# Kernel optimization log

Hardware: AMD Instinct MI355X
Metric: run time of the kernel (lower is better)

Reference implementation:

```python
import jax, jax.numpy as jnp
import numpy as np

T, C, NH, NL, NP = 5, 192, 4, 5, 4
DH = C // NH

def leaky(x):
    return jnp.where(x >= 0, x, 0.1 * x)

def conv2d(x, w, b, padding=1, dilation=1):
    out = jax.lax.conv_general_dilated(
        x, w, window_strides=(1, 1),
        padding=[(padding, padding), (padding, padding)],
        rhs_dilation=(dilation, dilation),
        dimension_numbers=('NCHW', 'OIHW', 'NCHW'))
    return out + b[None, :, None, None]

def grid_sample_border(img, gx, gy):
    # align_corners=True, padding_mode='border'; gx/gy normalized [-1,1], shape (B,H,W)
    B, Cc, H, W = img.shape
    x = jnp.clip((gx + 1.0) * 0.5 * (W - 1), 0.0, W - 1)
    y = jnp.clip((gy + 1.0) * 0.5 * (H - 1), 0.0, H - 1)
    x0 = jnp.floor(x); y0 = jnp.floor(y)
    wx = (x - x0).reshape(B, 1, -1); wy = (y - y0).reshape(B, 1, -1)
    flat = img.reshape(B, Cc, H * W)
    def g(yi, xi):
        xi = jnp.clip(xi, 0, W - 1).astype(jnp.int32)
        yi = jnp.clip(yi, 0, H - 1).astype(jnp.int32)
        return jnp.take_along_axis(flat, (yi * W + xi).reshape(B, 1, -1), axis=2)
    out = (g(y0, x0) * (1 - wx) * (1 - wy) + g(y0, x0 + 1) * wx * (1 - wy)
         + g(y0 + 1, x0) * (1 - wx) * wy + g(y0 + 1, x0 + 1) * wx * wy)
    return out.reshape(B, Cc, H, W)

def warp(x, flo):
    B, _, H, W = x.shape
    xx = jnp.arange(W, dtype=jnp.float32)[None, :] * jnp.ones((H, 1), jnp.float32)
    yy = jnp.arange(H, dtype=jnp.float32)[:, None] * jnp.ones((1, W), jnp.float32)
    gx = 2.0 * (xx[None] + flo[:, 0]) / max(W - 1, 1) - 1.0
    gy = 2.0 * (yy[None] + flo[:, 1]) / max(H - 1, 1) - 1.0
    return grid_sample_border(x, gx, gy)

def deform_sample(v_img, loc):
    # v_img (N,D,H,W); loc (N,Q,P,2) in [0,1]; bilinear, zeros padding, align_corners=False
    N, D, H, W = v_img.shape
    Q, P = loc.shape[1], loc.shape[2]
    x = loc[..., 0] * W - 0.5
    y = loc[..., 1] * H - 0.5
    x0 = jnp.floor(x); y0 = jnp.floor(y)
    wx = (x - x0).reshape(N, 1, -1); wy = (y - y0).reshape(N, 1, -1)
    flat = v_img.reshape(N, D, H * W)
    def g(yi, xi):
        valid = ((xi >= 0) & (xi <= W - 1) & (yi >= 0) & (yi <= H - 1)).astype(v_img.dtype)
        xi_c = jnp.clip(xi, 0, W - 1).astype(jnp.int32)
        yi_c = jnp.clip(yi, 0, H - 1).astype(jnp.int32)
        return jnp.take_along_axis(flat, (yi_c * W + xi_c).reshape(N, 1, -1), axis=2) * valid.reshape(N, 1, -1)
    out = (g(y0, x0) * (1 - wx) * (1 - wy) + g(y0, x0 + 1) * wx * (1 - wy)
         + g(y0 + 1, x0) * (1 - wx) * wy + g(y0 + 1, x0 + 1) * wx * wy)
    return out.reshape(N, D, Q, P)

def _forward(frame, srcframe, flow_forward, flow_backward,
             w_qk, b_qk, w_v, b_v, w_vproj, b_vproj, w_off, b_off,
             w_attn, b_attn, w_out, b_out, w_ff, b_ff,
             w_ffn1, b_ffn1, w_ffn2, b_ffn2):
    b, t, c, h, w = frame.shape
    ff01, ff12 = flow_forward[:, 0], flow_forward[:, 1]
    fb32, fb43 = flow_backward[:, 2], flow_backward[:, 3]
    ff02 = ff01 + warp(ff12, ff01)
    fb42 = fb43 + warp(fb32, fb43)
    warp02 = warp(frame[:, 0], ff02)
    warp12 = warp(frame[:, 1], ff12)
    warp32 = warp(frame[:, 3], fb32)
    warp42 = warp(frame[:, 4], fb42)
    qk_in = jnp.concatenate([warp02, warp12, frame[:, 2], warp32, warp42,
                             flow_forward.reshape(b, -1, h, w),
                             flow_backward.reshape(b, -1, h, w)], axis=1)
    queries = leaky(conv2d(qk_in, w_qk, b_qk)).reshape(b, t, c, h, w)
    value = leaky(conv2d(frame.reshape(b, t * c, h, w), w_v, b_v)).reshape(b, t, c, h, w)

    Lq = t * h * w
    q_tok = queries.transpose(0, 1, 3, 4, 2).reshape(b, Lq, c)
    v_tok = value.transpose(0, 1, 3, 4, 2).reshape(b, Lq, c)
    v_proj = (v_tok @ w_vproj.T + b_vproj).reshape(b, t, h * w, NH, DH)

    offs = (q_tok @ w_off.T + b_off).reshape(b, Lq, NH, NL, NP, 2)
    aw = (q_tok @ w_attn.T + b_attn).reshape(b, Lq, NH, NL * NP)
    aw = jax.nn.softmax(aw, axis=-1).reshape(b, Lq, NH, NL, NP)

    # reference points (all valid ratios are ones): ((x+0.5)/W, (y+0.5)/H)
    rx = (jnp.arange(w, dtype=frame.dtype) + 0.5) / w
    ry = (jnp.arange(h, dtype=frame.dtype) + 0.5) / h
    ref = jnp.stack(jnp.meshgrid(rx, ry, indexing='xy'), axis=-1).reshape(h * w, 2)
    ref = jnp.tile(ref, (t, 1))  # (Lq, 2)

    norm = jnp.array([w, h], dtype=frame.dtype)
    # flow-guided per-level displacement toward the center frame (level 2)
    zero = jnp.zeros_like(ff12)
    flows = jnp.stack([ff02, ff12, zero, fb32, fb42], axis=1)  # (b,NL,2,h,w)
    flow_norm = (flows / norm[None, None, :, None, None]).transpose(0, 1, 3, 4, 2).reshape(b, NL, h * w, 2)
    flow_norm = jnp.tile(flow_norm.transpose(0, 2, 1, 3), (1, t, 1, 1))  # (b,Lq,NL,2)

    loc = (ref[None, :, None, None, None, :]
           + offs / norm[None, None, None, None, None, :]
           + flow_norm[:, :, None, :, None, :])  # (b,Lq,NH,NL,NP,2)

    acc = jnp.zeros((b * NH, DH, Lq), dtype=frame.dtype)
    for l in range(NL):
        v_l = v_proj[:, l].transpose(0, 2, 3, 1).reshape(b * NH, DH, h, w)
        loc_l = loc[:, :, :, l].transpose(0, 2, 1, 3, 4).reshape(b * NH, Lq, NP, 2)
        samp = deform_sample(v_l, loc_l)  # (b*NH, DH, Lq, NP)
        w_l = aw[:, :, :, l].transpose(0, 2, 1, 3).reshape(b * NH, 1, Lq, NP)
        acc = acc + (samp * w_l).sum(-1)
    attn = acc.reshape(b, NH, DH, Lq).transpose(0, 3, 1, 2).reshape(b, Lq, c)
    attn = attn @ w_out.T + b_out

    out = attn.reshape(b, t, h, w, c).transpose(0, 1, 4, 2, 3).reshape(b * t, c, h, w)
    out = conv2d(out, w_ff, b_ff)
    out = out.reshape(b, t, c, h, w) + frame
    seq_in = jnp.concatenate([out.reshape(b * t, c, h, w), srcframe.reshape(b * t, c, h, w)], axis=1)
    ffn = conv2d(seq_in, w_ffn1, b_ffn1, padding=2, dilation=2)
    ffn = conv2d(leaky(ffn), w_ffn2, b_ffn2)
    out = out.reshape(b * t, c, h, w) + ffn
    return out.reshape(b, t, c, h, w)

def setup_inputs():
    key = jax.random.key(0)
    ks = jax.random.split(key, 16)
    B, H, W = 2, 64, 64
    s = 0.02
    d = {}
    d['frame'] = jax.random.normal(ks[0], (B, T, C, H, W), jnp.float32)
    d['srcframe'] = jax.random.normal(ks[1], (B, T, C, H, W), jnp.float32)
    d['flow_forward'] = jax.random.normal(ks[2], (B, 4, 2, H, W), jnp.float32)
    d['flow_backward'] = jax.random.normal(ks[3], (B, 4, 2, H, W), jnp.float32)
    cin_qk = T * C + 4 * (T - 1)
    d['w_qk'] = jax.random.normal(ks[4], (T * C, cin_qk, 3, 3), jnp.float32) * s
    d['b_qk'] = jnp.zeros((T * C,), jnp.float32)
    d['w_v'] = jax.random.normal(ks[5], (T * C, T * C, 3, 3), jnp.float32) * s
    d['b_v'] = jnp.zeros((T * C,), jnp.float32)
    d['w_vproj'] = jax.random.normal(ks[6], (C, C), jnp.float32) * s
    d['b_vproj'] = jnp.zeros((C,), jnp.float32)
    d['w_off'] = jax.random.normal(ks[7], (NH * NL * NP * 2, C), jnp.float32) * s
    d['b_off'] = jax.random.normal(ks[8], (NH * NL * NP * 2,), jnp.float32)
    d['w_attn'] = jax.random.normal(ks[9], (NH * NL * NP, C), jnp.float32) * s
    d['b_attn'] = jnp.zeros((NH * NL * NP,), jnp.float32)
    d['w_out'] = jax.random.normal(ks[10], (C, C), jnp.float32) * s
    d['b_out'] = jnp.zeros((C,), jnp.float32)
    d['w_ff'] = jax.random.normal(ks[11], (C, C, 3, 3), jnp.float32) * s
    d['b_ff'] = jnp.zeros((C,), jnp.float32)
    d['w_ffn1'] = jax.random.normal(ks[12], (C, 2 * C, 3, 3), jnp.float32) * s
    d['b_ffn1'] = jnp.zeros((C,), jnp.float32)
    d['w_ffn2'] = jax.random.normal(ks[13], (C, C, 3, 3), jnp.float32) * s
    d['b_ffn2'] = jnp.zeros((C,), jnp.float32)
    return d

def reference(frame, srcframe, flow_forward, flow_backward, w_qk, b_qk, w_v, b_v, w_vproj, b_vproj, w_off, b_off, w_attn, b_attn, w_out, b_out, w_ff, b_ff, w_ffn1, b_ffn1, w_ffn2, b_ffn2):
    out = _forward(frame, srcframe, flow_forward, flow_backward, w_qk, b_qk, w_v, b_v, w_vproj, b_vproj, w_off, b_off, w_attn, b_attn, w_out, b_out, w_ff, b_ff, w_ffn1, b_ffn1, w_ffn2, b_ffn2)
    return (out, srcframe)
```

## Files before the change

### kernel.cpp

```cpp
#include <hip/hip_runtime.h>


#define HWPX 4096
#define PPXN 4624
#define LQ   20480

typedef __attribute__((ext_vector_type(8))) short  short8;
typedef __attribute__((ext_vector_type(4))) short  short4v;
typedef __attribute__((ext_vector_type(4))) float  f32x4;

__device__ __forceinline__ unsigned short f2bf(float f) {
    unsigned u = __float_as_uint(f);
    unsigned r = (u + 0x7FFF + ((u >> 16) & 1)) >> 16;
    return (unsigned short)r;
}
__device__ __forceinline__ float bf2f(unsigned short s) {
    return __uint_as_float(((unsigned)s) << 16);
}

__device__ __forceinline__ void gl_lds16(const unsigned short* g, unsigned short* l) {
    __builtin_amdgcn_global_load_lds(
        (const __attribute__((address_space(1))) unsigned int*)g,
        (__attribute__((address_space(3))) unsigned int*)l, 16, 0, 0);
}

__device__ __forceinline__ float bsample(const float* __restrict__ p, float sx, float sy) {
    sx = fminf(fmaxf(sx, 0.f), 63.f);
    sy = fminf(fmaxf(sy, 0.f), 63.f);
    float x0 = floorf(sx), y0 = floorf(sy);
    int ix0 = (int)x0, iy0 = (int)y0;
    int ix1 = ix0 < 63 ? ix0 + 1 : 63;
    int iy1 = iy0 < 63 ? iy0 + 1 : 63;
    float wx = sx - x0, wy = sy - y0;
    float v00 = p[iy0*64+ix0], v01 = p[iy0*64+ix1];
    float v10 = p[iy1*64+ix0], v11 = p[iy1*64+ix1];
    return (v00*(1.f-wx) + v01*wx)*(1.f-wy) + (v10*(1.f-wx) + v11*wx)*wy;
}

__global__ __launch_bounds__(256) void k_flow(const float* __restrict__ ff,
                                              const float* __restrict__ fb,
                                              float* __restrict__ flows) {
    int i = blockIdx.x*256 + threadIdx.x;
    int b = i >> 12, pix = i & 4095;
    int x = pix & 63, y = pix >> 6;
    const float* ff01 = ff + (size_t)(b*4+0)*2*HWPX;
    const float* ff12 = ff + (size_t)(b*4+1)*2*HWPX;
    const float* fb32 = fb + (size_t)(b*4+2)*2*HWPX;
    const float* fb43 = fb + (size_t)(b*4+3)*2*HWPX;
    float* F = flows + (size_t)b*5*2*HWPX;
    float ax = ff01[pix], ay = ff01[HWPX+pix];
    float sx = bsample(ff12,      (float)x+ax, (float)y+ay);
    float sy = bsample(ff12+HWPX, (float)x+ax, (float)y+ay);
    F[0*2*HWPX + pix]        = ax + sx;
    F[0*2*HWPX + HWPX + pix] = ay + sy;
    F[1*2*HWPX + pix]        = ff12[pix];
    F[1*2*HWPX + HWPX + pix] = ff12[HWPX+pix];
    F[2*2*HWPX + pix]        = 0.f;
    F[2*2*HWPX + HWPX + pix] = 0.f;
    F[3*2*HWPX + pix]        = fb32[pix];
    F[3*2*HWPX + HWPX + pix] = fb32[HWPX+pix];
    float bx = fb43[pix], by = fb43[HWPX+pix];
    float tx = bsample(fb32,      (float)x+bx, (float)y+by);
    float ty = bsample(fb32+HWPX, (float)x+bx, (float)y+by);
    F[4*2*HWPX + pix]        = bx + tx;
    F[4*2*HWPX + HWPX + pix] = by + ty;
}

__global__ void k_qkin(const unsigned short* __restrict__ Pv,
                       const float* __restrict__ ff, const float* __restrict__ fb,
                       const float* __restrict__ flows,
                       unsigned short* __restrict__ Pqk)
{
    int ppx = blockIdx.x*64 + threadIdx.x;
    if (ppx >= PPXN) return;
    int b = blockIdx.z;
    int c8 = (blockIdx.y*4 + threadIdx.y)*8;
    unsigned short* dst = Pqk + ((size_t)b*PPXN + ppx)*992 + c8;
    int py = ppx/68, pxc = ppx - py*68;
    short8 o = {};
    if (py >= 2 && py < 66 && pxc >= 2 && pxc < 66 && c8 < 976) {
        int y = py-2, x = pxc-2, pix = (y<<6)+x;
        if (c8 >= 960) {
            #pragma unroll
            for (int j = 0; j < 8; ++j) {
                int k = c8 - 960 + j;
                float v = (k < 8) ? ff[((size_t)b*8 + k)*HWPX + pix]
                                  : fb[((size_t)b*8 + k - 8)*HWPX + pix];
                o[j] = (short)f2bf(v);
            }
        } else {
            const unsigned short* Pvb = Pv + (size_t)b*PPXN*960;
            int slot = c8/192;
            if (slot == 2) {
                o = *(const short8*)(Pvb + (size_t)ppx*960 + c8);
            } else {
                const float* F = flows + ((size_t)(b*5 + slot)*2)*HWPX;
                float sx = fminf(fmaxf((float)x + F[pix], 0.f), 63.f);
                float sy = fminf(fmaxf((float)y + F[HWPX + pix], 0.f), 63.f);
                float x0 = floorf(sx), y0 = floorf(sy);
                int ix0 = (int)x0, iy0 = (int)y0;
                int ix1 = ix0 < 63 ? ix0+1 : 63, iy1 = iy0 < 63 ? iy0+1 : 63;
                float wx = sx - x0, wy = sy - y0;
                float w00 = (1.f-wx)*(1.f-wy), w01 = wx*(1.f-wy);
                float w10 = (1.f-wx)*wy,       w11 = wx*wy;
                short8 v00 = *(const short8*)(Pvb + ((size_t)((iy0+2)*68 + ix0+2))*960 + c8);
                short8 v01 = *(const short8*)(Pvb + ((size_t)((iy0+2)*68 + ix1+2))*960 + c8);
                short8 v10 = *(const short8*)(Pvb + ((size_t)((iy1+2)*68 + ix0+2))*960 + c8);
                short8 v11 = *(const short8*)(Pvb + ((size_t)((iy1+2)*68 + ix1+2))*960 + c8);
                #pragma unroll
                for (int j = 0; j < 8; ++j) {
                    float v = bf2f((unsigned short)v00[j])*w00 + bf2f((unsigned short)v01[j])*w01
                            + bf2f((unsigned short)v10[j])*w10 + bf2f((unsigned short)v11[j])*w11;
                    o[j] = (short)f2bf(v);
                }
            }
        }
    }
    *(short8*)dst = o;
}

__global__ void t_pad(const float* __restrict__ in, unsigned short* __restrict__ outb,
                      int CI, int PITCH, int COFF)
{
    int ppx = blockIdx.x*64 + threadIdx.x;
    if (ppx >= PPXN) return;
    int img = blockIdx.z;
    int c8 = (blockIdx.y*4 + threadIdx.y)*8;
    unsigned short* dst = outb + ((size_t)img*PPXN + ppx)*PITCH;
    int py = ppx/68, pxc = ppx - py*68;
    if (py < 2 || py >= 66 || pxc < 2 || pxc >= 66) {
        short8 z = {};
        *(short8*)(dst + c8) = z;
        if (COFF) *(short8*)(dst + COFF + c8) = z;
        return;
    }
    int pix = ((py-2)<<6) + (pxc-2);
    short8 o;
    #pragma unroll
    for (int j = 0; j < 8; ++j)
        o[j] = (short)f2bf(in[((size_t)img*CI + c8 + j)*HWPX + pix]);
    *(short8*)(dst + COFF + c8) = o;
}

__global__ __launch_bounds__(256) void t_zb(unsigned short* __restrict__ b0,
                                            unsigned short* __restrict__ b1) {
    int id = blockIdx.x*256 + threadIdx.x;
    int ppx = id / 24, c8 = (id - ppx*24) * 8;
    if (ppx >= PPXN) return;
    int py = ppx/68, pxc = ppx - py*68;
    if (py >= 2 && py < 66 && pxc >= 2 && pxc < 66) return;
    int y = blockIdx.y;
    unsigned short* buf = (y < 10) ? b0 : b1;
    int img = (y < 10) ? y : y - 10;
    short8 z = {};
    *(short8*)(buf + ((size_t)img*PPXN + ppx)*192 + c8) = z;
}

__global__ __launch_bounds__(256) void t_wT(const float* __restrict__ w,
                                            unsigned short* __restrict__ wT,
                                            int CI, int NKB) {
    int cotile = blockIdx.x, kblk = blockIdx.y;
    int tid = threadIdx.x & 255;
    unsigned short* dst = wT + ((size_t)(cotile*NKB + kblk))*18432;
    #pragma unroll
    for (int it = 0; it < 9; ++it) {
        int idx = it*256 + tid;
        int tap = idx >> 8, sub = idx & 255;
        int cg = sub >> 6, co = sub & 63;
        int cog = cotile*64 + co;
        int ci0 = kblk*32 + cg*8;
        short8 v;
        #pragma unroll
        for (int j = 0; j < 8; ++j) {
            int ci = ci0 + j;
            v[j] = (ci < CI) ? (short)f2bf(w[((size_t)cog*CI + ci)*9 + tap]) : (short)0;
        }
        *(short8*)(dst + (size_t)idx*8) = v;
    }
}

__global__ __launch_bounds__(256) void t_wg(const float* __restrict__ w1,
                                            const float* __restrict__ w2,
                                            unsigned short* __restrict__ wg,
                                            int co_split, int CO) {
    int cotile = blockIdx.x;
    int tid = threadIdx.x & 255;
    unsigned short* dst = wg + (size_t)cotile*12288;
    #pragma unroll
    for (int it = 0; it < 6; ++it) {
        int idx = it*256 + tid;
        int kblk = idx >> 8, sub = idx & 255;
        int cg = sub >> 6, co = sub & 63;
        int cog = cotile*64 + co;
        int ci0 = kblk*32 + cg*8;
        short8 v = {};
        if (cog < CO) {
            const float* row = (cog < co_split) ? w1 + (size_t)cog*192
                                                : w2 + (size_t)(cog - co_split)*192;
            #pragma unroll
            for (int j = 0; j < 8; ++j) v[j] = (short)f2bf(row[ci0 + j]);
        }
        *(short8*)(dst + (size_t)idx*8) = v;
    }
}

template<int ROWS, int DIL, int OUTK, bool LEAKY, int RESK>
__global__ __launch_bounds__(256, 2) void k_conv(
    const unsigned short* __restrict__ P0, const unsigned short* __restrict__ P1,
    int CIP0, int CIP1, int NKB0, int NKB1,
    const unsigned short* __restrict__ wT0, const unsigned short* __restrict__ wT1,
    const float* __restrict__ bias0, const float* __restrict__ bias1,
    const float* __restrict__ resF, const unsigned short* __restrict__ resB, int resPitch,
    float* __restrict__ outF,
    unsigned short* __restrict__ outB0, unsigned short* __restrict__ outB1,
    int outPitch, int outCoff, int njobs)
{
    constexpr int RR     = ROWS*4 + 2*DIL;
    constexpr int XP     = 64 + 2*DIL;
    constexpr int PLANE  = RR*XP*16;
    constexpr int NCH    = RR*XP*4;
    constexpr int NXS    = (NCH + 255)/256;
    constexpr int TILEPX = ROWS*4*64;
    constexpr int SMEM_K = 4*PLANE + 36864;
    constexpr int SMEM_E = (OUTK <= 1) ? TILEPX*72*2 : 0;
    constexpr int SMEMSZ = SMEM_K > SMEM_E ? SMEM_K : SMEM_E;
    __shared__ __align__(16) unsigned char smem[SMEMSZ];
    unsigned char*  s_x = smem;
    unsigned short* s_w = (unsigned short*)(smem + 4*PLANE);

    int tid = threadIdx.x & 255;
    int gx = gridDim.x, gy = gridDim.y, gz = gridDim.z;
    int lin = blockIdx.x + gx*(blockIdx.y + gy*blockIdx.z);
    int tot = gx*gy*gz;
    if ((tot & 7) == 0) { int q = tot >> 3; lin = (lin & 7)*q + (lin >> 3); }
    int cotile = lin % gx; int rem = lin / gx;
    int ytile = rem % gy;  int z = rem / gy;

    int sel = (njobs == 2) ? (z >> 1) : 0;
    int img = (njobs == 2) ? (z & 1)  : z;
    const unsigned short* P  = sel ? P1  : P0;
    const unsigned short* wT = sel ? wT1 : wT0;
    const float* bias        = sel ? bias1 : bias0;
    unsigned short* outB     = sel ? outB1 : outB0;
    int CIP = sel ? CIP1 : CIP0;
    int NKB = sel ? NKB1 : NKB0;

    int y0 = ytile * (ROWS*4);
    const unsigned short* Pi = P + (size_t)img*PPXN*CIP;
    int w = tid >> 6, lane = tid & 63, lm = lane & 15, cig = lane >> 4;

    auto stage_x = [&](int kb) {
        int k0 = kb*32;
        #pragma unroll
        for (int it = 0; it < NXS; ++it) {
            int li = it*256 + tid;
            if (li < NCH) {
                int p = li / (RR*XP), rm = li - p*(RR*XP);
                int r = rm / XP, c = rm - r*XP;
                gl_lds16(Pi + ((size_t)((y0 + 2 - DIL + r)*68 + c + 2 - DIL))*CIP + k0 + p*8,
                         (unsigned short*)(s_x + li*16));
            }
        }
    };
    auto stage_w = [&](int kb) {
        const unsigned short* ws = wT + ((size_t)(cotile*NKB + kb))*18432;
        #pragma unroll
        for (int it = 0; it < 9; ++it)
            gl_lds16(ws + (size_t)(it*256+tid)*8, &s_w[(it*256+tid)*8]);
    };

    stage_x(0); stage_w(0);
    __syncthreads();

    f32x4 acc[4][ROWS*4] = {};
    for (int kb = 0; kb < NKB; ++kb) {
        __builtin_amdgcn_s_setprio(1);
        #pragma unroll
        for (int t = 0; t < 9; ++t) {
            int ky = t/3, kx = t - ky*3;
            short8 A[4];
            #pragma unroll
            for (int mb = 0; mb < 4; ++mb)
                A[mb] = *(const short8*)&s_w[((t*4 + cig)*64 + mb*16 + lm)*8];
            #pragma unroll
            for (int s = 0; s < ROWS; ++s) {
                short8 Bf[4];
                #pragma unroll
                for (int nc = 0; nc < 4; ++nc)
                    Bf[nc] = *(const short8*)&s_x[cig*PLANE +
                               ((w*ROWS + s + ky*DIL)*XP + nc*16 + lm + kx*DIL)*16];
                #pragma unroll
                for (int mb = 0; mb < 4; ++mb)
                    #pragma unroll
                    for (int nc = 0; nc < 4; ++nc)
                        acc[mb][s*4+nc] = __builtin_amdgcn_mfma_f32_16x16x32_bf16(
                            A[mb], Bf[nc], acc[mb][s*4+nc], 0, 0, 0);
            }
        }
        __builtin_amdgcn_s_setprio(0);
        __syncthreads();
        if (kb + 1 < NKB) { stage_x(kb+1); stage_w(kb+1); }
        __syncthreads();
    }

    if (OUTK == 0 || OUTK == 1) {
        unsigned short* epi = (unsigned short*)smem;
        #pragma unroll
        for (int mb = 0; mb < 4; ++mb) {
            int cob = cotile*64 + mb*16 + cig*4;
            int col = mb*16 + cig*4;
            #pragma unroll
            for (int s = 0; s < ROWS; ++s) {
                int lr = w*ROWS + s;
                #pragma unroll
                for (int nc = 0; nc < 4; ++nc) {
                    int x = nc*16 + lm;
                    int px_l = lr*64 + x;
                    int gpx = y0*64 + px_l;
                    short4v sv;
                    #pragma unroll
                    for (int r = 0; r < 4; ++r) {
                        float v = acc[mb][s*4+nc][r] + bias[cob + r];
                        if (LEAKY) v = v >= 0.f ? v : 0.1f*v;
                        if (RESK == 1) v += resF[((size_t)img*192 + cob + r)*HWPX + gpx];
                        sv[r] = (short)f2bf(v);
                    }
                    *(short4v*)&epi[px_l*72 + col] = sv;
                }
            }
        }
        __syncthreads();
        constexpr int NCPY = TILEPX/32;
        int slot = (OUTK == 0) ? (cotile*64)/192 : 0;
        int ccb  = (OUTK == 0) ? (cotile*64)%192 : (cotile*64 + outCoff);
        #pragma unroll
        for (int it2 = 0; it2 < NCPY; ++it2) {
            int li = it2*256 + tid;
            int px_l = li >> 3, sub = li & 7;
            short8 v = *(const short8*)&epi[px_l*72 + sub*8];
            int gpx = y0*64 + px_l;
            if (OUTK == 0) {
                *(short8*)(outB + ((size_t)(img*5 + slot)*HWPX + gpx)*192 + ccb + sub*8) = v;
            } else {
                int ppx = ((gpx>>6)+2)*68 + (gpx&63) + 2;
                *(short8*)(outB0 + ((size_t)img*PPXN + ppx)*outPitch + ccb + sub*8) = v;
            }
        }
    } else {
        #pragma unroll
        for (int mb = 0; mb < 4; ++mb) {
            int cob = cotile*64 + mb*16 + cig*4;
            #pragma unroll
            for (int s = 0; s < ROWS; ++s) {
                int y = y0 + w*ROWS + s;
                #pragma unroll
                for (int nc = 0; nc < 4; ++nc) {
                    int x = nc*16 + lm;
                    int px = (y<<6) + x;
                    int ppx = (y+2)*68 + x + 2;
                    short4v rv;
                    if (RESK == 2)
                        rv = *(const short4v*)(resB + ((size_t)img*PPXN + ppx)*resPitch + cob);
                    #pragma unroll
                    for (int r = 0; r < 4; ++r) {
                        float v = acc[mb][s*4+nc][r] + bias[cob + r];
                        if (LEAKY) v = v >= 0.f ? v : 0.1f*v;
                        if (RESK == 1) v += resF[((size_t)img*192 + cob + r)*HWPX + px];
                        if (RESK == 2) v += bf2f((unsigned short)rv[r]);
                        outF[((size_t)img*192 + cob + r)*HWPX + px] = v;
                    }
                }
            }
        }
    }
}

template<int GMODE>
__global__ __launch_bounds__(256) void k_gemmm(
    const unsigned short* __restrict__ X, const unsigned short* __restrict__ WG,
    const float* __restrict__ b1, const float* __restrict__ b2,
    float* __restrict__ o1, float* __restrict__ o2, unsigned short* __restrict__ ob)
{
    __shared__ unsigned char  s_x[2][4*4096];
    __shared__ unsigned short s_w[12288];
    int tid = threadIdx.x & 255;
    int cotile = blockIdx.x, pxt = blockIdx.y, img = blockIdx.z;
    int px0 = pxt*256;
    const unsigned short* Xi = X + (size_t)img*HWPX*192;
    #pragma unroll
    for (int it = 0; it < 6; ++it)
        gl_lds16(WG + (size_t)cotile*12288 + (it*256+tid)*8, &s_w[(it*256+tid)*8]);
    short8 xr[4];
    #pragma unroll
    for (int it = 0; it < 4; ++it)
        xr[it] = *(const short8*)(Xi + (size_t)(px0 + tid)*192 + it*8);
    #pragma unroll
    for (int it = 0; it < 4; ++it)
        *(short8*)&s_x[0][it*4096 + tid*16] = xr[it];
    __syncthreads();
    int w = tid >> 6, lane = tid & 63, lm = lane & 15, cig = lane >> 4;
    f32x4 acc[4][4] = {};
    int xb = 0;
    for (int kb = 0; kb < 6; ++kb) {
        bool pf = (kb < 5);
        if (pf) {
            int k0 = (kb+1)*32;
            #pragma unroll
            for (int it = 0; it < 4; ++it)
                xr[it] = *(const short8*)(Xi + (size_t)(px0 + tid)*192 + k0 + it*8);
        }
        short8 A[4], Bf[4];
        #pragma unroll
        for (int nb = 0; nb < 4; ++nb)
            Bf[nb] = *(const short8*)&s_x[xb][cig*4096 + (w*64 + nb*16 + lm)*16];
        #pragma unroll
        for (int mb = 0; mb < 4; ++mb)
            A[mb] = *(const short8*)&s_w[((kb*4 + cig)*64 + mb*16 + lm)*8];
        #pragma unroll
        for (int mb = 0; mb < 4; ++mb)
            #pragma unroll
            for (int nb = 0; nb < 4; ++nb)
                acc[mb][nb] = __builtin_amdgcn_mfma_f32_16x16x32_bf16(
                    A[mb], Bf[nb], acc[mb][nb], 0, 0, 0);
        if (pf) {
            #pragma unroll
            for (int it = 0; it < 4; ++it)
                *(short8*)&s_x[xb^1][it*4096 + tid*16] = xr[it];
        }
        __syncthreads();
        xb ^= 1;
    }
    int b = img/5, t = img - b*5;
    #pragma unroll
    for (int mb = 0; mb < 4; ++mb) {
        int cob = cotile*64 + mb*16 + cig*4;
        if (GMODE == 1 && cob >= 240) continue;
        #pragma unroll
        for (int nb = 0; nb < 4; ++nb) {
            int px = px0 + w*64 + nb*16 + lm;
            float vv[4];
            #pragma unroll
            for (int r = 0; r < 4; ++r) {
                float bv;
                if (GMODE == 1) bv = (cob + r < 160) ? b1[cob+r] : b2[cob+r-160];
                else bv = b1[cob + r];
                vv[r] = acc[mb][nb][r] + bv;
            }
            if (GMODE == 0) {
                int h = cob/48, d = cob - h*48;
                short4v s;
                #pragma unroll
                for (int r = 0; r < 4; ++r) s[r] = (short)f2bf(vv[r]);
                *(short4v*)(ob + (((size_t)img*4 + h)*HWPX + px)*48 + d) = s;
            } else if (GMODE == 1) {
                #pragma unroll
                for (int r = 0; r < 4; ++r) {
                    int co = cob + r;
                    if (co < 160) o1[((size_t)b*160 + co)*LQ + t*HWPX + px] = vv[r];
                    else          o2[((size_t)b*80 + co-160)*LQ + t*HWPX + px] = vv[r];
                }
            } else {
                int ppx = ((px>>6)+2)*68 + (px&63) + 2;
                short4v s;
                #pragma unroll
                for (int r = 0; r < 4; ++r) s[r] = (short)f2bf(vv[r]);
                *(short4v*)(ob + ((size_t)img*PPXN + ppx)*192 + cob) = s;
            }
        }
    }
}

__device__ __forceinline__ void addtap(float* acc, const unsigned short* __restrict__ src, float w) {
    const short8* s8 = (const short8*)src;
    #pragma unroll
    for (int q = 0; q < 6; ++q) {
        short8 v = s8[q];
        #pragma unroll
        for (int j = 0; j < 8; ++j)
            acc[q*8+j] += w * bf2f((unsigned short)v[j]);
    }
}

__global__ __launch_bounds__(256) void k_sample(
    const unsigned short* __restrict__ vp, const float* __restrict__ offs,
    const float* __restrict__ aw, const float* __restrict__ flows,
    unsigned short* __restrict__ accout)
{
    int blk = blockIdx.x;
    int b = blk / 320, sub = blk - b*320;
    int h = threadIdx.x >> 6;
    int lq = sub*64 + (threadIdx.x & 63);
    int pix = lq & 4095;
    int x = pix & 63, y = pix >> 6;
    const float* offp = offs + ((size_t)b*160 + h*40)*LQ + lq;
    const float* awp  = aw   + ((size_t)b*80  + h*20)*LQ + lq;
    float e[20];
    float m = -1e30f;
    #pragma unroll
    for (int j = 0; j < 20; ++j) { e[j] = awp[(size_t)j*LQ]; m = fmaxf(m, e[j]); }
    float ssum = 0.f;
    #pragma unroll
    for (int j = 0; j < 20; ++j) { e[j] = __expf(e[j]-m); ssum += e[j]; }
    float inv = 1.f/ssum;

    float acc[48];
    #pragma unroll
    for (int d = 0; d < 48; ++d) acc[d] = 0.f;

    for (int l = 0; l < 5; ++l) {
        float fx = flows[((size_t)(b*5+l)*2+0)*HWPX + pix];
        float fy = flows[((size_t)(b*5+l)*2+1)*HWPX + pix];
        const unsigned short* vpl = vp + ((size_t)(b*5+l)*4 + h)*HWPX*48;
        #pragma unroll
        for (int p = 0; p < 4; ++p) {
            int o = l*4 + p;
            float ox = offp[(size_t)(2*o)*LQ];
            float oy = offp[(size_t)(2*o+1)*LQ];
            float wv = e[o]*inv;
            float sx = (float)x + ox + fx;
            float sy = (float)y + oy + fy;
            float x0f = floorf(sx), y0f = floorf(sy);
            float wx = sx - x0f, wy = sy - y0f;
            int ix0 = (int)x0f, iy0 = (int)y0f;
            float w00 = wv*(1.f-wx)*(1.f-wy), w01 = wv*wx*(1.f-wy);
            float w10 = wv*(1.f-wx)*wy,       w11 = wv*wx*wy;
            bool vx0 = (ix0 >= 0)  && (ix0 <= 63);
            bool vx1 = (ix0 >= -1) && (ix0 <= 62);
            bool vy0 = (iy0 >= 0)  && (iy0 <= 63);
            bool vy1 = (iy0 >= -1) && (iy0 <= 62);
            if (vy0 && vx0) addtap(acc, vpl + (size_t)(iy0*64 + ix0)*48,       w00);
            if (vy0 && vx1) addtap(acc, vpl + (size_t)(iy0*64 + ix0 + 1)*48,   w01);
            if (vy1 && vx0) addtap(acc, vpl + (size_t)((iy0+1)*64 + ix0)*48,   w10);
            if (vy1 && vx1) addtap(acc, vpl + (size_t)((iy0+1)*64 + ix0+1)*48, w11);
        }
    }
    unsigned short* dst = accout + ((size_t)b*LQ + lq)*192 + h*48;
    #pragma unroll
    for (int q = 0; q < 6; ++q) {
        short8 s;
        #pragma unroll
        for (int j = 0; j < 8; ++j) s[j] = (short)f2bf(acc[q*8+j]);
        *(short8*)(dst + q*8) = s;
    }
}


extern "C" void kernel_launch(void* const* d_in, const int* in_sizes, int n_in,
                              void* d_out, int out_size, void* d_ws, size_t ws_size,
                              hipStream_t stream) {
    (void)in_sizes; (void)n_in; (void)out_size; (void)ws_size;
    const float* frame    = (const float*)d_in[0];
    const float* srcframe = (const float*)d_in[1];
    const float* flow_f   = (const float*)d_in[2];
    const float* flow_b   = (const float*)d_in[3];
    const float* w_qk  = (const float*)d_in[4];  const float* b_qk  = (const float*)d_in[5];
    const float* w_v   = (const float*)d_in[6];  const float* b_v   = (const float*)d_in[7];
    const float* w_vp  = (const float*)d_in[8];  const float* b_vp  = (const float*)d_in[9];
    const float* w_off = (const float*)d_in[10]; const float* b_off = (const float*)d_in[11];
    const float* w_at  = (const float*)d_in[12]; const float* b_at  = (const float*)d_in[13];
    const float* w_out = (const float*)d_in[14]; const float* b_out = (const float*)d_in[15];
    const float* w_ff  = (const float*)d_in[16]; const float* b_ff  = (const float*)d_in[17];
    const float* w_f1  = (const float*)d_in[18]; const float* b_f1  = (const float*)d_in[19];
    const float* w_f2  = (const float*)d_in[20]; const float* b_f2  = (const float*)d_in[21];
    float* out = (float*)d_out;
    char* W = (char*)d_ws;

    float*          flows  = (float*)(W + 0);
    unsigned short* wT_qk  = (unsigned short*)(W + 327680);
    unsigned short* wT_v   = (unsigned short*)(W + 17469440);
    unsigned short* wT_ff  = (unsigned short*)(W + 327680);
    unsigned short* wT_f1  = (unsigned short*)(W + 991232);
    unsigned short* wT_f2  = (unsigned short*)(W + 2318336);
    unsigned short* wg_vp  = (unsigned short*)(W + 2981888);
    unsigned short* wg_oa  = (unsigned short*)(W + 3055616);
    unsigned short* wg_out = (unsigned short*)(W + 3153920);
    unsigned short* P_qk   = (unsigned short*)(W + 34058240);
    unsigned short* P_ff   = P_qk;
    unsigned short* P_v    = (unsigned short*)(W + 52406272);
    unsigned short* P_mid  = P_v;
    unsigned short* Q_tok  = (unsigned short*)(W + 70162432);
    unsigned short* acc_tok= Q_tok;
    unsigned short* V_tok  = (unsigned short*)(W + 85891072);
    unsigned short* P_ffn1 = V_tok;
    unsigned short* vp     = (unsigned short*)(W + 101619712);
    float*          offs   = (float*)(W + 121403392);
    float*          aw     = (float*)(W + 147617792);

    dim3 bp(64, 4);

    k_flow<<<32, 256, 0, stream>>>(flow_f, flow_b, flows);
    t_wT<<<dim3(15,31), 256, 0, stream>>>(w_qk, wT_qk, 976, 31);
    t_wT<<<dim3(15,30), 256, 0, stream>>>(w_v,  wT_v,  960, 30);
    t_pad<<<dim3(73,30,2), bp, 0, stream>>>(frame, P_v, 960, 960, 0);
    k_qkin<<<dim3(73,31,2), bp, 0, stream>>>(P_v, flow_f, flow_b, flows, P_qk);
    k_conv<2,1,0,true,0><<<dim3(15,8,4), 256, 0, stream>>>(
        P_qk, P_v, 992, 960, 31, 30, wT_qk, wT_v, b_qk, b_v,
        nullptr, nullptr, 0, nullptr, Q_tok, V_tok, 0, 0, 2);
    t_wT<<<dim3(3,6),  256, 0, stream>>>(w_ff, wT_ff, 192, 6);
    t_wT<<<dim3(3,12), 256, 0, stream>>>(w_f1, wT_f1, 384, 12);
    t_wT<<<dim3(3,6),  256, 0, stream>>>(w_f2, wT_f2, 192, 6);
    t_wg<<<3, 256, 0, stream>>>(w_vp,  nullptr, wg_vp, 192, 192);
    t_wg<<<4, 256, 0, stream>>>(w_off, w_at,    wg_oa, 160, 240);
    t_wg<<<3, 256, 0, stream>>>(w_out, nullptr, wg_out, 192, 192);
    t_zb<<<dim3(434,20), 256, 0, stream>>>(P_ff, P_mid);
    k_gemmm<0><<<dim3(3,16,10), 256, 0, stream>>>(V_tok, wg_vp, b_vp, nullptr,
                                                  nullptr, nullptr, vp);
    k_gemmm<1><<<dim3(4,16,10), 256, 0, stream>>>(Q_tok, wg_oa, b_off, b_at,
                                                  offs, aw, nullptr);
    k_sample<<<640, 256, 0, stream>>>(vp, offs, aw, flows, acc_tok);
    t_pad<<<dim3(73,6,10), bp, 0, stream>>>(srcframe, P_ffn1, 192, 384, 192);
    k_gemmm<2><<<dim3(3,16,10), 256, 0, stream>>>(acc_tok, wg_out, b_out, nullptr,
                                                  nullptr, nullptr, P_ff);
    k_conv<1,1,1,false,1><<<dim3(3,16,10), 256, 0, stream>>>(
        P_ff, nullptr, 192, 0, 6, 0, wT_ff, nullptr, b_ff, nullptr,
        frame, nullptr, 0, nullptr, P_ffn1, nullptr, 384, 0, 1);
    k_conv<1,2,1,true,0><<<dim3(3,16,10), 256, 0, stream>>>(
        P_ffn1, nullptr, 384, 0, 12, 0, wT_f1, nullptr, b_f1, nullptr,
        nullptr, nullptr, 0, nullptr, P_mid, nullptr, 192, 0, 1);
    k_conv<1,1,2,false,2><<<dim3(3,16,10), 256, 0, stream>>>(
        P_mid, nullptr, 192, 0, 6, 0, wT_f2, nullptr, b_f2, nullptr,
        nullptr, P_ffn1, 384, out, nullptr, nullptr, 0, 0, 1);
    hipMemcpyAsync(out + (size_t)2*5*192*HWPX, srcframe,
                   (size_t)2*5*192*HWPX*sizeof(float),
                   hipMemcpyDeviceToDevice, stream);
}
```

Before: 939.2 us.

## Coalesce weight transpose, pad conv LDS planes, merge projection GEMMs into one launch

The weight-transpose kernel now stages 32 output channels of fp32 weights in shared memory with contiguous reads, then packs bf16 from there, replacing the strided scattered global loads. The conv kernel pads each input-channel plane in LDS by 32 bytes and the GEMM input buffers by 32 bytes per plane, aiming to reduce LDS bank conflicts on the MFMA operand reads. The value-projection and offset/attention GEMMs are fused into one launch with a 7-wide grid, cutting one launch and letting the two run concurrently. The padding chunks are filled with dummy loads, which adds a little extra load traffic.

```diff
diff --git a/kernel.cpp b/kernel.cpp
--- a/kernel.cpp
+++ b/kernel.cpp
@@ -159,23 +159,33 @@
 __global__ __launch_bounds__(256) void t_wT(const float* __restrict__ w,
                                             unsigned short* __restrict__ wT,
                                             int CI, int NKB) {
+    __shared__ float s[32][289];
     int cotile = blockIdx.x, kblk = blockIdx.y;
     int tid = threadIdx.x & 255;
     unsigned short* dst = wT + ((size_t)(cotile*NKB + kblk))*18432;
-    #pragma unroll
-    for (int it = 0; it < 9; ++it) {
-        int idx = it*256 + tid;
-        int tap = idx >> 8, sub = idx & 255;
-        int cg = sub >> 6, co = sub & 63;
-        int cog = cotile*64 + co;
-        int ci0 = kblk*32 + cg*8;
-        short8 v;
-        #pragma unroll
-        for (int j = 0; j < 8; ++j) {
-            int ci = ci0 + j;
-            v[j] = (ci < CI) ? (short)f2bf(w[((size_t)cog*CI + ci)*9 + tap]) : (short)0;
-        }
-        *(short8*)(dst + (size_t)idx*8) = v;
+    int ci0 = kblk*32;
+    int navail = CI - ci0; if (navail > 32) navail = 32;
+    for (int half = 0; half < 2; ++half) {
+        int co_base = half*32;
+        for (int li = tid; li < 32*288; li += 256) {
+            int co_l = li / 288, f = li - co_l*288;
+            int ci_l = f / 9;
+            float v = 0.f;
+            if (ci_l < navail)
+                v = w[((size_t)(cotile*64 + co_base + co_l)*CI + ci0)*9 + f];
+            s[co_l][f] = v;
+        }
+        __syncthreads();
+        for (int li = tid; li < 9*4*32; li += 256) {
+            int tap = li / 128, rem2 = li - tap*128;
+            int cg = rem2 >> 5, co_l = rem2 & 31;
+            short8 v;
+            #pragma unroll
+            for (int j = 0; j < 8; ++j)
+                v[j] = (short)f2bf(s[co_l][(cg*8+j)*9 + tap]);
+            *(short8*)(dst + ((size_t)(tap*256 + cg*64 + co_base + co_l))*8) = v;
+        }
+        __syncthreads();
     }
 }
 
@@ -215,18 +225,20 @@
     unsigned short* __restrict__ outB0, unsigned short* __restrict__ outB1,
     int outPitch, int outCoff, int njobs)
 {
-    constexpr int RR     = ROWS*4 + 2*DIL;
-    constexpr int XP     = 64 + 2*DIL;
-    constexpr int PLANE  = RR*XP*16;
-    constexpr int NCH    = RR*XP*4;
-    constexpr int NXS    = (NCH + 255)/256;
-    constexpr int TILEPX = ROWS*4*64;
-    constexpr int SMEM_K = 4*PLANE + 36864;
-    constexpr int SMEM_E = (OUTK <= 1) ? TILEPX*72*2 : 0;
-    constexpr int SMEMSZ = SMEM_K > SMEM_E ? SMEM_K : SMEM_E;
+    constexpr int RR      = ROWS*4 + 2*DIL;
+    constexpr int XP      = 64 + 2*DIL;
+    constexpr int PLANE   = RR*XP*16;
+    constexpr int PSTRIDE = PLANE + 32;
+    constexpr int CPP     = PSTRIDE/16;
+    constexpr int NCHP    = 4*CPP;
+    constexpr int NXS     = (NCHP + 255)/256;
+    constexpr int TILEPX  = ROWS*4*64;
+    constexpr int SMEM_K  = 4*PSTRIDE + 36864;
+    constexpr int SMEM_E  = (OUTK <= 1) ? TILEPX*72*2 : 0;
+    constexpr int SMEMSZ  = SMEM_K > SMEM_E ? SMEM_K : SMEM_E;
     __shared__ __align__(16) unsigned char smem[SMEMSZ];
     unsigned char*  s_x = smem;
-    unsigned short* s_w = (unsigned short*)(smem + 4*PLANE);
+    unsigned short* s_w = (unsigned short*)(smem + 4*PSTRIDE);
 
     int tid = threadIdx.x & 255;
     int gx = gridDim.x, gy = gridDim.y, gz = gridDim.z;
@@ -254,11 +266,14 @@
         #pragma unroll
         for (int it = 0; it < NXS; ++it) {
             int li = it*256 + tid;
-            if (li < NCH) {
-                int p = li / (RR*XP), rm = li - p*(RR*XP);
-                int r = rm / XP, c = rm - r*XP;
-                gl_lds16(Pi + ((size_t)((y0 + 2 - DIL + r)*68 + c + 2 - DIL))*CIP + k0 + p*8,
-                         (unsigned short*)(s_x + li*16));
+            if (li < NCHP) {
+                int p = li / CPP, rm = li - p*CPP;
+                const unsigned short* src = Pi;
+                if (rm < RR*XP) {
+                    int r = rm / XP, c = rm - r*XP;
+                    src = Pi + ((size_t)((y0 + 2 - DIL + r)*68 + c + 2 - DIL))*CIP + k0 + p*8;
+                }
+                gl_lds16(src, (unsigned short*)(s_x + li*16));
             }
         }
     };
@@ -287,7 +302,7 @@
                 short8 Bf[4];
                 #pragma unroll
                 for (int nc = 0; nc < 4; ++nc)
-                    Bf[nc] = *(const short8*)&s_x[cig*PLANE +
+                    Bf[nc] = *(const short8*)&s_x[cig*PSTRIDE +
                                ((w*ROWS + s + ky*DIL)*XP + nc*16 + lm + kx*DIL)*16];
                 #pragma unroll
                 for (int mb = 0; mb < 4; ++mb)
@@ -375,97 +390,118 @@
     }
 }
 
-template<int GMODE>
-__global__ __launch_bounds__(256) void k_gemmm(
+#define GEMM_BODY(Xi, WG_, cotile_)                                              \
+    __shared__ unsigned char  s_x[2][4*4128];                                    \
+    __shared__ unsigned short s_w[12288];                                        \
+    int tid = threadIdx.x & 255;                                                 \
+    _Pragma("unroll")                                                            \
+    for (int it = 0; it < 6; ++it)                                               \
+        gl_lds16(WG_ + (size_t)(cotile_)*12288 + (it*256+tid)*8,                 \
+                 &s_w[(it*256+tid)*8]);                                          \
+    short8 xr[4];                                                                \
+    _Pragma("unroll")                                                            \
+    for (int it = 0; it < 4; ++it)                                               \
+        xr[it] = *(const short8*)(Xi + (size_t)(px0 + tid)*192 + it*8);          \
+    _Pragma("unroll")                                                            \
+    for (int it = 0; it < 4; ++it)                                               \
+        *(short8*)&s_x[0][it*4128 + tid*16] = xr[it];                            \
+    __syncthreads();                                                             \
+    int w = tid >> 6, lane = tid & 63, lm = lane & 15, cig = lane >> 4;          \
+    f32x4 acc[4][4] = {};                                                        \
+    int xb = 0;                                                                  \
+    for (int kb = 0; kb < 6; ++kb) {                                             \
+        bool pf = (kb < 5);                                                      \
+        if (pf) {                                                                \
+            int k0 = (kb+1)*32;                                                  \
+            _Pragma("unroll")                                                    \
+            for (int it = 0; it < 4; ++it)                                       \
+                xr[it] = *(const short8*)(Xi + (size_t)(px0 + tid)*192 + k0 + it*8); \
+        }                                                                        \
+        short8 A[4], Bf[4];                                                      \
+        _Pragma("unroll")                                                        \
+        for (int nb = 0; nb < 4; ++nb)                                           \
+            Bf[nb] = *(const short8*)&s_x[xb][cig*4128 + (w*64 + nb*16 + lm)*16];\
+        _Pragma("unroll")                                                        \
+        for (int mb = 0; mb < 4; ++mb)                                           \
+            A[mb] = *(const short8*)&s_w[((kb*4 + cig)*64 + mb*16 + lm)*8];      \
+        _Pragma("unroll")                                                        \
+        for (int mb = 0; mb < 4; ++mb)                                           \
+            _Pragma("unroll")                                                    \
+            for (int nb = 0; nb < 4; ++nb)                                       \
+                acc[mb][nb] = __builtin_amdgcn_mfma_f32_16x16x32_bf16(           \
+                    A[mb], Bf[nb], acc[mb][nb], 0, 0, 0);                        \
+        if (pf) {                                                                \
+            _Pragma("unroll")                                                    \
+            for (int it = 0; it < 4; ++it)                                       \
+                *(short8*)&s_x[xb^1][it*4128 + tid*16] = xr[it];                 \
+        }                                                                        \
+        __syncthreads();                                                         \
+        xb ^= 1;                                                                 \
+    }
+
+__global__ __launch_bounds__(256) void k_gemm_pair(
+    const unsigned short* __restrict__ Xv, const unsigned short* __restrict__ WGv,
+    const float* __restrict__ bvp, unsigned short* __restrict__ vp,
+    const unsigned short* __restrict__ Xq, const unsigned short* __restrict__ WGq,
+    const float* __restrict__ boff, const float* __restrict__ batt,
+    float* __restrict__ offs, float* __restrict__ aw)
+{
+    int bx = blockIdx.x, pxt = blockIdx.y, img = blockIdx.z;
+    int px0 = pxt*256;
+    bool isv = bx < 3;
+    int cotile = isv ? bx : bx - 3;
+    const unsigned short* Xi = (isv ? Xv : Xq) + (size_t)img*HWPX*192;
+    const unsigned short* WG = isv ? WGv : WGq;
+    GEMM_BODY(Xi, WG, cotile)
+    int b = img/5, t = img - b*5;
+    #pragma unroll
+    for (int mb = 0; mb < 4; ++mb) {
+        int cob = cotile*64 + mb*16 + cig*4;
+        if (!isv && cob >= 240) continue;
+        #pragma unroll
+        for (int nb = 0; nb < 4; ++nb) {
+            int px = px0 + w*64 + nb*16 + lm;
+            if (isv) {
+                int h = cob/48, d = cob - h*48;
+                short4v s;
+                #pragma unroll
+                for (int r = 0; r < 4; ++r)
+                    s[r] = (short)f2bf(acc[mb][nb][r] + bvp[cob + r]);
+                *(short4v*)(vp + (((size_t)img*4 + h)*HWPX + px)*48 + d) = s;
+            } else {
+                #pragma unroll
+                for (int r = 0; r < 4; ++r) {
+                    int co = cob + r;
+                    float bv = (co < 160) ? boff[co] : batt[co-160];
+                    float v = acc[mb][nb][r] + bv;
+                    if (co < 160) offs[((size_t)b*160 + co)*LQ + t*HWPX + px] = v;
+                    else          aw[((size_t)b*80 + co-160)*LQ + t*HWPX + px] = v;
+                }
+            }
+        }
+    }
+}
+
+__global__ __launch_bounds__(256) void k_gemm_out(
     const unsigned short* __restrict__ X, const unsigned short* __restrict__ WG,
-    const float* __restrict__ b1, const float* __restrict__ b2,
-    float* __restrict__ o1, float* __restrict__ o2, unsigned short* __restrict__ ob)
+    const float* __restrict__ b1, unsigned short* __restrict__ ob)
 {
-    __shared__ unsigned char  s_x[2][4*4096];
-    __shared__ unsigned short s_w[12288];
-    int tid = threadIdx.x & 255;
     int cotile = blockIdx.x, pxt = blockIdx.y, img = blockIdx.z;
     int px0 = pxt*256;
     const unsigned short* Xi = X + (size_t)img*HWPX*192;
-    #pragma unroll
-    for (int it = 0; it < 6; ++it)
-        gl_lds16(WG + (size_t)cotile*12288 + (it*256+tid)*8, &s_w[(it*256+tid)*8]);
-    short8 xr[4];
-    #pragma unroll
-    for (int it = 0; it < 4; ++it)
-        xr[it] = *(const short8*)(Xi + (size_t)(px0 + tid)*192 + it*8);
-    #pragma unroll
-    for (int it = 0; it < 4; ++it)
-        *(short8*)&s_x[0][it*4096 + tid*16] = xr[it];
-    __syncthreads();
-    int w = tid >> 6, lane = tid & 63, lm = lane & 15, cig = lane >> 4;
-    f32x4 acc[4][4] = {};
-    int xb = 0;
-    for (int kb = 0; kb < 6; ++kb) {
-        bool pf = (kb < 5);
-        if (pf) {
-            int k0 = (kb+1)*32;
-            #pragma unroll
-            for (int it = 0; it < 4; ++it)
-                xr[it] = *(const short8*)(Xi + (size_t)(px0 + tid)*192 + k0 + it*8);
-        }
-        short8 A[4], Bf[4];
-        #pragma unroll
-        for (int nb = 0; nb < 4; ++nb)
-            Bf[nb] = *(const short8*)&s_x[xb][cig*4096 + (w*64 + nb*16 + lm)*16];
-        #pragma unroll
-        for (int mb = 0; mb < 4; ++mb)
-            A[mb] = *(const short8*)&s_w[((kb*4 + cig)*64 + mb*16 + lm)*8];
-        #pragma unroll
-        for (int mb = 0; mb < 4; ++mb)
-            #pragma unroll
-            for (int nb = 0; nb < 4; ++nb)
-                acc[mb][nb] = __builtin_amdgcn_mfma_f32_16x16x32_bf16(
-                    A[mb], Bf[nb], acc[mb][nb], 0, 0, 0);
-        if (pf) {
-            #pragma unroll
-            for (int it = 0; it < 4; ++it)
-                *(short8*)&s_x[xb^1][it*4096 + tid*16] = xr[it];
-        }
-        __syncthreads();
-        xb ^= 1;
-    }
-    int b = img/5, t = img - b*5;
+    GEMM_BODY(Xi, WG, cotile)
     #pragma unroll
     for (int mb = 0; mb < 4; ++mb) {
         int cob = cotile*64 + mb*16 + cig*4;
-        if (GMODE == 1 && cob >= 240) continue;
         #pragma unroll
         for (int nb = 0; nb < 4; ++nb) {
             int px = px0 + w*64 + nb*16 + lm;
-            float vv[4];
-            #pragma unroll
-            for (int r = 0; r < 4; ++r) {
-                float bv;
-                if (GMODE == 1) bv = (cob + r < 160) ? b1[cob+r] : b2[cob+r-160];
-                else bv = b1[cob + r];
-                vv[r] = acc[mb][nb][r] + bv;
-            }
-            if (GMODE == 0) {
-                int h = cob/48, d = cob - h*48;
-                short4v s;
-                #pragma unroll
-                for (int r = 0; r < 4; ++r) s[r] = (short)f2bf(vv[r]);
-                *(short4v*)(ob + (((size_t)img*4 + h)*HWPX + px)*48 + d) = s;
-            } else if (GMODE == 1) {
-                #pragma unroll
-                for (int r = 0; r < 4; ++r) {
-                    int co = cob + r;
-                    if (co < 160) o1[((size_t)b*160 + co)*LQ + t*HWPX + px] = vv[r];
-                    else          o2[((size_t)b*80 + co-160)*LQ + t*HWPX + px] = vv[r];
-                }
-            } else {
-                int ppx = ((px>>6)+2)*68 + (px&63) + 2;
-                short4v s;
-                #pragma unroll
-                for (int r = 0; r < 4; ++r) s[r] = (short)f2bf(vv[r]);
-                *(short4v*)(ob + ((size_t)img*PPXN + ppx)*192 + cob) = s;
-            }
+            int ppx = ((px>>6)+2)*68 + (px&63) + 2;
+            short4v s;
+            #pragma unroll
+            for (int r = 0; r < 4; ++r)
+                s[r] = (short)f2bf(acc[mb][nb][r] + b1[cob + r]);
+            *(short4v*)(ob + ((size_t)img*PPXN + ppx)*192 + cob) = s;
         }
     }
 }
@@ -603,14 +639,11 @@
     t_wg<<<4, 256, 0, stream>>>(w_off, w_at,    wg_oa, 160, 240);
     t_wg<<<3, 256, 0, stream>>>(w_out, nullptr, wg_out, 192, 192);
     t_zb<<<dim3(434,20), 256, 0, stream>>>(P_ff, P_mid);
-    k_gemmm<0><<<dim3(3,16,10), 256, 0, stream>>>(V_tok, wg_vp, b_vp, nullptr,
-                                                  nullptr, nullptr, vp);
-    k_gemmm<1><<<dim3(4,16,10), 256, 0, stream>>>(Q_tok, wg_oa, b_off, b_at,
-                                                  offs, aw, nullptr);
+    k_gemm_pair<<<dim3(7,16,10), 256, 0, stream>>>(
+        V_tok, wg_vp, b_vp, vp, Q_tok, wg_oa, b_off, b_at, offs, aw);
     k_sample<<<640, 256, 0, stream>>>(vp, offs, aw, flows, acc_tok);
     t_pad<<<dim3(73,6,10), bp, 0, stream>>>(srcframe, P_ffn1, 192, 384, 192);
-    k_gemmm<2><<<dim3(3,16,10), 256, 0, stream>>>(acc_tok, wg_out, b_out, nullptr,
-                                                  nullptr, nullptr, P_ff);
+    k_gemm_out<<<dim3(3,16,10), 256, 0, stream>>>(acc_tok, wg_out, b_out, P_ff);
     k_conv<1,1,1,false,1><<<dim3(3,16,10), 256, 0, stream>>>(
         P_ff, nullptr, 192, 0, 6, 0, wT_ff, nullptr, b_ff, nullptr,
         frame, nullptr, 0, nullptr, P_ffn1, nullptr, 384, 0, 1);
```

Result: slower. 994.7 us (+5.9%).
